# Kernel tuning notes

Measured on AMD Instinct MI355X. Metric: run time of the kernel, lower is better.

## Reference

```python
import jax, jax.numpy as jnp
import numpy as np

N_GRAPHS = 500
NODES_PER_GRAPH = 200
EDGES_PER_GRAPH = 6400
N = N_GRAPHS * NODES_PER_GRAPH          # 100000 nodes
E = N_GRAPHS * EDGES_PER_GRAPH          # 3200000 edges
D = 256                                  # dim_hidden
RATIO = 0.8
EPS = 1e-12


def setup_inputs() -> dict:
    key = jax.random.key(0)
    k1, k2 = jax.random.split(key, 2)
    x = jax.random.normal(k1, (N, D), dtype=jnp.float32)
    # edges consistent with batch: both endpoints inside the same graph
    rng = np.random.default_rng(0)
    g = np.repeat(np.arange(N_GRAPHS, dtype=np.int32), EDGES_PER_GRAPH)
    row = g * NODES_PER_GRAPH + rng.integers(0, NODES_PER_GRAPH, E).astype(np.int32)
    col = g * NODES_PER_GRAPH + rng.integers(0, NODES_PER_GRAPH, E).astype(np.int32)
    edge_index = jnp.asarray(np.stack([row, col]), dtype=jnp.int32)
    batch = jnp.asarray(np.repeat(np.arange(N_GRAPHS, dtype=np.int32), NODES_PER_GRAPH))
    W = jax.random.normal(k2, (2 * D, 1), dtype=jnp.float32) * (1.0 / np.sqrt(2 * D))
    b = jnp.zeros((1,), dtype=jnp.float32)
    return {"x": x, "edge_index": edge_index, "batch": batch, "W": W, "b": b}


def _edge_scores(x, W, b, edge_index):
    # concat(x[row], x[col]) @ W == (x @ W_row)[row] + (x @ W_col)[col]
    # -> avoids materializing the [E, 2D] edge_rep tensor.
    row, col = edge_index[0], edge_index[1]
    s_row = x @ W[:D, 0]   # [N]
    s_col = x @ W[D:, 0]   # [N]
    return s_row[row] + s_col[col] + b[0]  # [E]


def _topk_edge_mask(edge_score, edge_graph):
    # sparse_sort (descending=True): norm = minmax(score) - graph_id; argsort desc.
    f_min, f_max = edge_score.min(), edge_score.max()
    norm = (edge_score - f_min) / (f_max - f_min + EPS) - edge_graph.astype(edge_score.dtype)
    perm = jnp.argsort(-norm)  # graphs ascending, score descending within graph
    deg = jax.ops.segment_sum(jnp.ones_like(edge_graph), edge_graph, num_segments=N_GRAPHS)
    k = jnp.ceil(RATIO * deg.astype(jnp.float32)).astype(deg.dtype)
    start = jnp.concatenate([jnp.zeros((1,), deg.dtype), jnp.cumsum(deg)[:-1]])
    sg = edge_graph[perm]                        # graph id in sorted order
    pos = jnp.arange(E, dtype=deg.dtype) - start[sg]  # rank within segment
    keep_sorted = pos < k[sg]
    # scatter keep flags back to original edge order
    return jnp.zeros((E,), dtype=bool).at[perm].set(keep_sorted)


def _relabel(x, batch, edge_index, emask):
    # padded equivalent of torch.unique + scatter relabel:
    # selected nodes are compacted to the front of x/batch; dropped slots -> -1.
    row, col = edge_index[0], edge_index[1]
    m = emask.astype(jnp.int32)
    sel = (jnp.zeros((N,), jnp.int32).at[row].max(m).at[col].max(m)).astype(bool)
    new_id = jnp.where(sel, jnp.cumsum(sel) - 1, -1)           # [N]
    new_ei = jnp.where(emask[None, :], new_id[edge_index], -1)  # [2, E], -1 = padding
    order = jnp.argsort(~sel)                                   # stable: selected first
    x_out = x[order]                                            # [N, D], selected at front
    batch_out = jnp.where(sel[order], batch[order], -1)
    return x_out, new_ei, batch_out, sel.sum()


def reference(x, edge_index, batch, W, b):
    edge_score = _edge_scores(x, W, b, edge_index)
    edge_graph = batch[edge_index[0]]
    mask = _topk_edge_mask(edge_score, edge_graph)   # True = causal edge
    causal_w = jnp.where(mask, edge_score, 0.0)
    conf_w = jnp.where(mask, 0.0, -edge_score)
    causal_x, causal_ei, causal_batch, n_causal = _relabel(x, batch, edge_index, mask)
    conf_x, conf_ei, conf_batch, n_conf = _relabel(x, batch, edge_index, ~mask)
    return (causal_x, causal_ei, causal_w, causal_batch, n_causal,
            conf_x, conf_ei, conf_w, conf_batch, n_conf,
            edge_score, mask)
```

## Files before the change

### kernel.cpp

```cpp
#include <hip/hip_runtime.h>
#include <cmath>

typedef unsigned long long u64;
typedef unsigned int u32;
typedef unsigned char u8;

#define DHID 256
#define NMAX 100000
#define EMAX 3200000
#define EPGMAX 6400
#define NPG 200
#define GMAX 512
#define TOPK_T 1024

__device__ float  g_srow[NMAX];
__device__ float  g_scol[NMAX];
__device__ uchar2 g_lei[EMAX];
__device__ u8     g_mask[EMAX];
__device__ u8     g_selC[NMAX];
__device__ u8     g_selF[NMAX];
__device__ float  g_pmin[GMAX];
__device__ float  g_pmax[GMAX];
__device__ int    g_cntC[GMAX];
__device__ int    g_cntF[GMAX];
__device__ int    g_offC[GMAX];
__device__ int    g_offF[GMAX];
__device__ int    g_tot[2];

__global__ __launch_bounds__(256) void k_scores(const float* __restrict__ x,
    const int* __restrict__ ei, const float* __restrict__ W, const float* __restrict__ b,
    float* __restrict__ out, long long oS, int E, int N){
  __shared__ float srow_l[NPG], scol_l[NPG];
  __shared__ float smin[4], smax[4];
  int g = blockIdx.x, tid = threadIdx.x;
  int lane = tid & 63, wid = tid >> 6;
  int nbase = g * NPG;

  float4 wr = ((const float4*)W)[lane];
  float4 wc = ((const float4*)W)[64 + lane];
  for (int it = 0; it < NPG/4; it++){
    int n0 = it*4 + wid;
    int n = nbase + n0;
    float4 xv = ((const float4*)(x + (size_t)n*DHID))[lane];
    double dr = (double)xv.x*wr.x + (double)xv.y*wr.y + (double)xv.z*wr.z + (double)xv.w*wr.w;
    double dc = (double)xv.x*wc.x + (double)xv.y*wc.y + (double)xv.z*wc.z + (double)xv.w*wc.w;
    #pragma unroll
    for (int off = 32; off; off >>= 1){
      dr += __shfl_xor(dr, off);
      dc += __shfl_xor(dc, off);
    }
    if (lane == 0){ srow_l[n0] = (float)dr; scol_l[n0] = (float)dc; }
  }
  __syncthreads();
  if (tid < NPG){
    g_srow[nbase + tid] = srow_l[tid];
    g_scol[nbase + tid] = scol_l[tid];
  }

  float b0 = b[0];
  float lmin = INFINITY, lmax = -INFINITY;
  long long ebase = (long long)g * EPGMAX;
  for (int it = 0; it < EPGMAX/256; it++){
    long long e = ebase + it*256 + tid;
    int r0 = ei[e]     - nbase;
    int c0 = ei[E + e] - nbase;
    r0 = min(max(r0, 0), NPG-1);
    c0 = min(max(c0, 0), NPG-1);
    float s = (srow_l[r0] + scol_l[c0]) + b0;
    uchar2 rc; rc.x = (u8)r0; rc.y = (u8)c0;
    g_lei[e] = rc;
    out[oS + e] = s;
    lmin = fminf(lmin, s); lmax = fmaxf(lmax, s);
  }
  #pragma unroll
  for (int off = 32; off; off >>= 1){
    lmin = fminf(lmin, __shfl_xor(lmin, off));
    lmax = fmaxf(lmax, __shfl_xor(lmax, off));
  }
  if (lane == 0){ smin[wid] = lmin; smax[wid] = lmax; }
  __syncthreads();
  if (tid == 0){
    g_pmin[g] = fminf(fminf(smin[0], smin[1]), fminf(smin[2], smin[3]));
    g_pmax[g] = fmaxf(fmaxf(smax[0], smax[1]), fmaxf(smax[2], smax[3]));
  }
}

__global__ __launch_bounds__(TOPK_T) void k_topk(const float* __restrict__ b,
    float* __restrict__ out, long long oCW, long long oFW, long long oM,
    int E, int EPG, int k){
  __shared__ u32 keys[EPGMAX];
  __shared__ u8  keep[EPGMAX];
  __shared__ float srow_l[NPG], scol_l[NPG];
  __shared__ u8 selC_l[NPG], selF_l[NPG];
  __shared__ int hist[256];
  __shared__ float wred[16], wred2[16];
  __shared__ int wsum[16];
  __shared__ u32 sh_prefix;
  __shared__ int sh_rem, sh_rem_next, sh_digit;
  int g = blockIdx.x, tid = threadIdx.x;
  int lane = tid & 63, wid = tid >> 6;
  int G = (int)gridDim.x;
  int nbase = g * NPG;
  long long base = (long long)g * EPG;

  if (tid < NPG){
    srow_l[tid] = g_srow[nbase + tid];
    scol_l[tid] = g_scol[nbase + tid];
    selC_l[tid] = 0; selF_l[tid] = 0;
  }

  float lmin = (tid < G) ? g_pmin[tid] : INFINITY;
  float lmax = (tid < G) ? g_pmax[tid] : -INFINITY;
  #pragma unroll
  for (int off = 32; off; off >>= 1){
    lmin = fminf(lmin, __shfl_xor(lmin, off));
    lmax = fmaxf(lmax, __shfl_xor(lmax, off));
  }
  if (lane == 0){ wred[wid] = lmin; wred2[wid] = lmax; }
  if (tid == 0){ sh_prefix = 0; sh_rem = k; }
  __syncthreads();
  float fmin = wred[0], fmax = wred2[0];
  #pragma unroll
  for (int w = 1; w < 16; w++){
    fmin = fminf(fmin, wred[w]); fmax = fmaxf(fmax, wred2[w]);
  }

  float b0 = b[0];
  float denom = (fmax - fmin) + 1e-12f;
  float gf = (float)g;

  for (int i = tid; i < EPG; i += TOPK_T){
    uchar2 rc = g_lei[base + i];
    float s = (srow_l[rc.x] + scol_l[rc.y]) + b0;
    float frac = (s - fmin) / denom;
    float nk = frac - gf;
    u32 u = __float_as_uint(nk);
    u = (u & 0x80000000u) ? ~u : (u | 0x80000000u);
    keys[i] = ~u;
  }
  for (int shift = 24; shift >= 0; shift -= 8){
    if (tid < 256) hist[tid] = 0;
    __syncthreads();
    u32 pref = sh_prefix;
    for (int i = tid; i < EPG; i += TOPK_T){
      u32 kk = keys[i];
      bool cand = (shift == 24) || ((kk >> (shift + 8)) == pref);
      if (cand){
        u32 digit = (kk >> shift) & 0xFF;
        u32 d0 = __builtin_amdgcn_readfirstlane(digit);
        if (__all(digit == d0)){
          u64 m = __ballot(1);
          if (lane == __builtin_ctzll(m)) atomicAdd(&hist[d0], (int)__popcll(m));
        } else {
          atomicAdd(&hist[digit], 1);
        }
      }
    }
    __syncthreads();
    int v = 0, inc = 0;
    if (tid < 256){
      v = hist[tid];
      inc = v;
      #pragma unroll
      for (int off = 1; off < 64; off <<= 1){
        int t2 = __shfl_up(inc, off);
        if (lane >= off) inc += t2;
      }
      if (lane == 63) wsum[wid] = inc;
    }
    __syncthreads();
    if (tid < 256){
      int wpre = 0;
      for (int w = 0; w < wid; w++) wpre += wsum[w];
      int incl = inc + wpre;
      int cumprev = incl - v;
      int rem = sh_rem;
      if (cumprev < rem && rem <= incl){
        sh_digit = tid;
        sh_rem_next = rem - cumprev;
      }
    }
    __syncthreads();
    if (tid == 0){
      sh_prefix = (sh_prefix << 8) | (u32)sh_digit;
      sh_rem = sh_rem_next;
    }
    __syncthreads();
  }
  u32 T = sh_prefix;
  int r_budget = sh_rem;

  int CH = (EPG + TOPK_T - 1) / TOPK_T;
  int c0 = tid * CH;
  int cnt = 0;
  for (int j = 0; j < CH; j++){
    int i = c0 + j;
    if (i < EPG && keys[i] == T) cnt++;
  }
  int inc2 = cnt;
  #pragma unroll
  for (int off = 1; off < 64; off <<= 1){
    int t2 = __shfl_up(inc2, off);
    if (lane >= off) inc2 += t2;
  }
  if (lane == 63) wsum[wid] = inc2;
  __syncthreads();
  int wpre2 = 0;
  for (int w = 0; w < wid; w++) wpre2 += wsum[w];
  int rank = inc2 - cnt + wpre2;

  for (int j = 0; j < CH; j++){
    int i = c0 + j;
    if (i >= EPG) break;
    u32 kk = keys[i];
    int kept;
    if (kk < T) kept = 1;
    else if (kk == T){ kept = (rank < r_budget); rank++; }
    else kept = 0;
    keep[i] = (u8)kept;
  }
  __syncthreads();

  for (int i = tid; i < EPG; i += TOPK_T){
    long long e = base + i;
    int kept = keep[i];
    uchar2 rc = g_lei[e];
    float s = (srow_l[rc.x] + scol_l[rc.y]) + b0;
    g_mask[e] = (u8)kept;
    out[oM + e]  = kept ? 1.0f : 0.0f;
    out[oCW + e] = kept ? s : 0.0f;
    out[oFW + e] = kept ? 0.0f : -s;
    if (kept){ selC_l[rc.x] = 1; selC_l[rc.y] = 1; }
    else     { selF_l[rc.x] = 1; selF_l[rc.y] = 1; }
  }
  __syncthreads();

  if (tid < NPG){
    g_selC[nbase + tid] = selC_l[tid];
    g_selF[nbase + tid] = selF_l[tid];
  }
  if (tid < 256){
    int vC = (tid < NPG) ? (int)selC_l[tid] : 0;
    int vF = (tid < NPG) ? (int)selF_l[tid] : 0;
    #pragma unroll
    for (int off = 32; off; off >>= 1){
      vC += __shfl_xor(vC, off); vF += __shfl_xor(vF, off);
    }
    if (lane == 0){ wsum[wid] = vC; wsum[8 + wid] = vF; }
  }
  __syncthreads();
  if (tid == 0){
    g_cntC[g] = wsum[0]+wsum[1]+wsum[2]+wsum[3];
    g_cntF[g] = wsum[8]+wsum[9]+wsum[10]+wsum[11];
  }
}

__global__ __launch_bounds__(GMAX) void k_scan(int G, float* __restrict__ out,
    long long oNC, long long oNF){
  __shared__ int wsC[8], wsF[8];
  int tid = threadIdx.x;
  int lane = tid & 63, wid = tid >> 6;
  int c = (tid < G) ? g_cntC[tid] : 0;
  int f = (tid < G) ? g_cntF[tid] : 0;
  int ic = c, iff = f;
  #pragma unroll
  for (int off = 1; off < 64; off <<= 1){
    int a = __shfl_up(ic, off), b2 = __shfl_up(iff, off);
    if (lane >= off){ ic += a; iff += b2; }
  }
  if (lane == 63){ wsC[wid] = ic; wsF[wid] = iff; }
  __syncthreads();
  int pc = 0, pf = 0;
  for (int w = 0; w < wid; w++){ pc += wsC[w]; pf += wsF[w]; }
  if (tid < G){ g_offC[tid] = ic - c + pc; g_offF[tid] = iff - f + pf; }
  if (tid == GMAX - 1){
    g_tot[0] = ic + pc; g_tot[1] = iff + pf;
    out[oNC] = (float)(ic + pc);
    out[oNF] = (float)(iff + pf);
  }
}

__global__ __launch_bounds__(256) void k_final(const float* __restrict__ x,
    float* __restrict__ out, long long oCX, long long oFX, long long oCE, long long oFE,
    long long oCB, long long oFB, int E, int N, int EPG){
  __shared__ int dC_l[NPG], dF_l[NPG];
  __shared__ int wsC[4], wsF[4];
  int g = blockIdx.x, tid = threadIdx.x;
  int lane = tid & 63, wid = tid >> 6;
  int nbase = g * NPG;
  long long ebase = (long long)g * EPG;

  int sC = (tid < NPG) ? (int)g_selC[nbase + tid] : 0;
  int sF = (tid < NPG) ? (int)g_selF[nbase + tid] : 0;
  int ic = sC, iff = sF;
  #pragma unroll
  for (int off = 1; off < 64; off <<= 1){
    int a = __shfl_up(ic, off), b2 = __shfl_up(iff, off);
    if (lane >= off){ ic += a; iff += b2; }
  }
  if (lane == 63){ wsC[wid] = ic; wsF[wid] = iff; }
  __syncthreads();
  int pc = 0, pf = 0;
  for (int w = 0; w < wid; w++){ pc += wsC[w]; pf += wsF[w]; }
  int cumC = ic + pc;
  int cumF = iff + pf;
  int offC = g_offC[g], offF = g_offF[g];
  int nC = g_tot[0], nF = g_tot[1];
  if (tid < NPG){
    int n = nbase + tid;
    int gCumC = offC + cumC;
    int gCumF = offF + cumF;
    int dC = sC ? (gCumC - 1) : (nC + (n - gCumC));
    int dF = sF ? (gCumF - 1) : (nF + (n - gCumF));
    dC = min(max(dC, 0), N-1);
    dF = min(max(dF, 0), N-1);
    dC_l[tid] = dC; dF_l[tid] = dF;
    float bt = (float)g;
    out[oCB + dC] = sC ? bt : -1.0f;
    out[oFB + dF] = sF ? bt : -1.0f;
  }
  __syncthreads();

  for (int it = 0; it < EPGMAX/256; it++){
    long long e = ebase + it*256 + tid;
    uchar2 rc = g_lei[e];
    int m = g_mask[e];
    out[oCE + e]     = m ? (float)dC_l[rc.x] : -1.0f;
    out[oCE + E + e] = m ? (float)dC_l[rc.y] : -1.0f;
    out[oFE + e]     = m ? -1.0f : (float)dF_l[rc.x];
    out[oFE + E + e] = m ? -1.0f : (float)dF_l[rc.y];
  }

  for (int it = 0; it < NPG/4; it++){
    int t = it*4 + wid;
    int n = nbase + t;
    float4 v = ((const float4*)(x + (size_t)n*DHID))[lane];
    int dC = dC_l[t], dF = dF_l[t];
    *reinterpret_cast<float4*>(out + oCX + (long long)dC*DHID + lane*4) = v;
    long long iF = oFX + (long long)dF*DHID + lane*4;
    out[iF] = v.x;
    float2 mid; mid.x = v.y; mid.y = v.z;
    *reinterpret_cast<float2*>(out + iF + 1) = mid;
    out[iF + 3] = v.w;
  }
}

extern "C" void kernel_launch(void* const* d_in, const int* in_sizes, int n_in,
                              void* d_out, int out_size, void* d_ws, size_t ws_size,
                              hipStream_t stream) {
  const float* x   = (const float*)d_in[0];
  const int* ei    = (const int*)d_in[1];
  const float* W   = (const float*)d_in[3];
  const float* b   = (const float*)d_in[4];
  float* out = (float*)d_out;

  int N   = in_sizes[0] / DHID;
  int E   = in_sizes[1] / 2;
  if (N > NMAX) N = NMAX;
  if (E > EMAX) E = EMAX;
  const int G   = N / NPG;
  int EPG = (G > 0) ? E / G : 0;
  if (EPG > EPGMAX) EPG = EPGMAX;
  const int k   = (int)ceilf(0.8f * (float)EPG);

  long long oCX = 0;
  long long oCE = oCX + (long long)N*DHID;
  long long oCW = oCE + 2LL*E;
  long long oCB = oCW + E;
  long long oNC = oCB + N;
  long long oFX = oNC + 1;
  long long oFE = oFX + (long long)N*DHID;
  long long oFW = oFE + 2LL*E;
  long long oFB = oFW + E;
  long long oNF = oFB + N;
  long long oS  = oNF + 1;
  long long oM  = oS + E;

  k_scores<<<G, 256, 0, stream>>>(x, ei, W, b, out, oS, E, N);
  k_topk<<<G, TOPK_T, 0, stream>>>(b, out, oCW, oFW, oM, E, EPG, k);
  k_scan<<<1, GMAX, 0, stream>>>(G, out, oNC, oNF);
  k_final<<<G, 256, 0, stream>>>(x, out, oCX, oFX, oCE, oFE, oCB, oFB, E, N, EPG);
}
```

Measured before the change: 161.5 us.

## Fuse graph-offset scan into final kernel and skip common radix digits in top-k

Removes the single-block scan kernel: each final block now reduces all per-graph counts itself to get its exclusive offset and the global totals, saving a launch and a serialization point. The final kernel moves to 512 threads. In top-k, the per-graph key min/max is reduced and the radix select starts at the highest byte where min and max differ, skipping histogram passes over leading bytes that all keys share. Every final block redundantly reads and reduces the count arrays, which adds some work per block.

```diff
diff --git a/kernel.cpp b/kernel.cpp
--- a/kernel.cpp
+++ b/kernel.cpp
@@ -23,9 +23,6 @@
 __device__ float  g_pmax[GMAX];
 __device__ int    g_cntC[GMAX];
 __device__ int    g_cntF[GMAX];
-__device__ int    g_offC[GMAX];
-__device__ int    g_offF[GMAX];
-__device__ int    g_tot[2];
 
 __global__ __launch_bounds__(256) void k_scores(const float* __restrict__ x,
     const int* __restrict__ ei, const float* __restrict__ W, const float* __restrict__ b,
@@ -95,6 +92,7 @@
   __shared__ int hist[256];
   __shared__ float wred[16], wred2[16];
   __shared__ int wsum[16];
+  __shared__ u32 wkmin[16], wkmax[16];
   __shared__ u32 sh_prefix;
   __shared__ int sh_rem, sh_rem_next, sh_digit;
   int g = blockIdx.x, tid = threadIdx.x;
@@ -117,7 +115,6 @@
     lmax = fmaxf(lmax, __shfl_xor(lmax, off));
   }
   if (lane == 0){ wred[wid] = lmin; wred2[wid] = lmax; }
-  if (tid == 0){ sh_prefix = 0; sh_rem = k; }
   __syncthreads();
   float fmin = wred[0], fmax = wred2[0];
   #pragma unroll
@@ -129,6 +126,7 @@
   float denom = (fmax - fmin) + 1e-12f;
   float gf = (float)g;
 
+  u32 ukmin = 0xFFFFFFFFu, ukmax = 0u;
   for (int i = tid; i < EPG; i += TOPK_T){
     uchar2 rc = g_lei[base + i];
     float s = (srow_l[rc.x] + scol_l[rc.y]) + b0;
@@ -136,15 +134,41 @@
     float nk = frac - gf;
     u32 u = __float_as_uint(nk);
     u = (u & 0x80000000u) ? ~u : (u | 0x80000000u);
-    keys[i] = ~u;
-  }
-  for (int shift = 24; shift >= 0; shift -= 8){
+    u32 kk = ~u;
+    keys[i] = kk;
+    ukmin = min(ukmin, kk); ukmax = max(ukmax, kk);
+  }
+  #pragma unroll
+  for (int off = 32; off; off >>= 1){
+    ukmin = min(ukmin, (u32)__shfl_xor((int)ukmin, off));
+    ukmax = max(ukmax, (u32)__shfl_xor((int)ukmax, off));
+  }
+  if (lane == 0){ wkmin[wid] = ukmin; wkmax[wid] = ukmax; }
+  __syncthreads();
+  u32 kmin = wkmin[0], kmax = wkmax[0];
+  #pragma unroll
+  for (int w = 1; w < 16; w++){
+    kmin = min(kmin, wkmin[w]); kmax = max(kmax, wkmax[w]);
+  }
+
+  u32 diff = kmin ^ kmax;
+  int startShift; u32 prefInit;
+  if (diff == 0){ startShift = -8; prefInit = kmin; }
+  else {
+    int sb = (31 - __clz(diff)) >> 3;
+    startShift = sb * 8;
+    prefInit = (sb == 3) ? 0u : (kmin >> ((sb+1)*8));
+  }
+  if (tid == 0){ sh_prefix = prefInit; sh_rem = k; }
+  __syncthreads();
+
+  for (int shift = startShift; shift >= 0; shift -= 8){
     if (tid < 256) hist[tid] = 0;
     __syncthreads();
     u32 pref = sh_prefix;
     for (int i = tid; i < EPG; i += TOPK_T){
       u32 kk = keys[i];
-      bool cand = (shift == 24) || ((kk >> (shift + 8)) == pref);
+      bool cand = (shift == startShift) || ((kk >> (shift + 8)) == pref);
       if (cand){
         u32 digit = (kk >> shift) & 0xFF;
         u32 d0 = __builtin_amdgcn_readfirstlane(digit);
@@ -255,41 +279,39 @@
   }
 }
 
-__global__ __launch_bounds__(GMAX) void k_scan(int G, float* __restrict__ out,
-    long long oNC, long long oNF){
-  __shared__ int wsC[8], wsF[8];
-  int tid = threadIdx.x;
-  int lane = tid & 63, wid = tid >> 6;
-  int c = (tid < G) ? g_cntC[tid] : 0;
-  int f = (tid < G) ? g_cntF[tid] : 0;
-  int ic = c, iff = f;
-  #pragma unroll
-  for (int off = 1; off < 64; off <<= 1){
-    int a = __shfl_up(ic, off), b2 = __shfl_up(iff, off);
-    if (lane >= off){ ic += a; iff += b2; }
-  }
-  if (lane == 63){ wsC[wid] = ic; wsF[wid] = iff; }
-  __syncthreads();
-  int pc = 0, pf = 0;
-  for (int w = 0; w < wid; w++){ pc += wsC[w]; pf += wsF[w]; }
-  if (tid < G){ g_offC[tid] = ic - c + pc; g_offF[tid] = iff - f + pf; }
-  if (tid == GMAX - 1){
-    g_tot[0] = ic + pc; g_tot[1] = iff + pf;
-    out[oNC] = (float)(ic + pc);
-    out[oNF] = (float)(iff + pf);
-  }
-}
-
-__global__ __launch_bounds__(256) void k_final(const float* __restrict__ x,
+__global__ __launch_bounds__(512) void k_final(const float* __restrict__ x,
     float* __restrict__ out, long long oCX, long long oFX, long long oCE, long long oFE,
-    long long oCB, long long oFB, int E, int N, int EPG){
+    long long oCB, long long oFB, long long oNC, long long oNF,
+    int E, int N, int EPG, int G){
   __shared__ int dC_l[NPG], dF_l[NPG];
+  __shared__ int wredA[8], wredB[8], wredC2[8], wredD[8];
   __shared__ int wsC[4], wsF[4];
   int g = blockIdx.x, tid = threadIdx.x;
   int lane = tid & 63, wid = tid >> 6;
   int nbase = g * NPG;
   long long ebase = (long long)g * EPG;
 
+  int vC = (tid < G) ? g_cntC[tid] : 0;
+  int vF = (tid < G) ? g_cntF[tid] : 0;
+  int mC = (tid < g) ? vC : 0;
+  int mF = (tid < g) ? vF : 0;
+  #pragma unroll
+  for (int off = 32; off; off >>= 1){
+    vC += __shfl_xor(vC, off); vF += __shfl_xor(vF, off);
+    mC += __shfl_xor(mC, off); mF += __shfl_xor(mF, off);
+  }
+  if (lane == 0){ wredA[wid] = vC; wredB[wid] = vF; wredC2[wid] = mC; wredD[wid] = mF; }
+  __syncthreads();
+  int nC = 0, nF = 0, offC = 0, offF = 0;
+  #pragma unroll
+  for (int w = 0; w < 8; w++){
+    nC += wredA[w]; nF += wredB[w]; offC += wredC2[w]; offF += wredD[w];
+  }
+  if (g == 0 && tid == 0){
+    out[oNC] = (float)nC;
+    out[oNF] = (float)nF;
+  }
+
   int sC = (tid < NPG) ? (int)g_selC[nbase + tid] : 0;
   int sF = (tid < NPG) ? (int)g_selF[nbase + tid] : 0;
   int ic = sC, iff = sF;
@@ -298,18 +320,14 @@
     int a = __shfl_up(ic, off), b2 = __shfl_up(iff, off);
     if (lane >= off){ ic += a; iff += b2; }
   }
-  if (lane == 63){ wsC[wid] = ic; wsF[wid] = iff; }
-  __syncthreads();
-  int pc = 0, pf = 0;
-  for (int w = 0; w < wid; w++){ pc += wsC[w]; pf += wsF[w]; }
-  int cumC = ic + pc;
-  int cumF = iff + pf;
-  int offC = g_offC[g], offF = g_offF[g];
-  int nC = g_tot[0], nF = g_tot[1];
+  if (lane == 63 && wid < 4){ wsC[wid] = ic; wsF[wid] = iff; }
+  __syncthreads();
   if (tid < NPG){
+    int pc = 0, pf = 0;
+    for (int w = 0; w < wid; w++){ pc += wsC[w]; pf += wsF[w]; }
+    int gCumC = offC + ic + pc;
+    int gCumF = offF + iff + pf;
     int n = nbase + tid;
-    int gCumC = offC + cumC;
-    int gCumF = offF + cumF;
     int dC = sC ? (gCumC - 1) : (nC + (n - gCumC));
     int dF = sF ? (gCumF - 1) : (nF + (n - gCumF));
     dC = min(max(dC, 0), N-1);
@@ -321,8 +339,8 @@
   }
   __syncthreads();
 
-  for (int it = 0; it < EPGMAX/256; it++){
-    long long e = ebase + it*256 + tid;
+  for (int i = tid; i < EPG; i += 512){
+    long long e = ebase + i;
     uchar2 rc = g_lei[e];
     int m = g_mask[e];
     out[oCE + e]     = m ? (float)dC_l[rc.x] : -1.0f;
@@ -331,8 +349,8 @@
     out[oFE + E + e] = m ? -1.0f : (float)dF_l[rc.y];
   }
 
-  for (int it = 0; it < NPG/4; it++){
-    int t = it*4 + wid;
+  for (int it = 0; it < NPG/8; it++){
+    int t = it*8 + wid;
     int n = nbase + t;
     float4 v = ((const float4*)(x + (size_t)n*DHID))[lane];
     int dC = dC_l[t], dF = dF_l[t];
@@ -378,6 +396,5 @@
 
   k_scores<<<G, 256, 0, stream>>>(x, ei, W, b, out, oS, E, N);
   k_topk<<<G, TOPK_T, 0, stream>>>(b, out, oCW, oFW, oM, E, EPG, k);
-  k_scan<<<1, GMAX, 0, stream>>>(G, out, oNC, oNF);
-  k_final<<<G, 256, 0, stream>>>(x, out, oCX, oFX, oCE, oFE, oCB, oFB, E, N, EPG);
+  k_final<<<G, 512, 0, stream>>>(x, out, oCX, oFX, oCE, oFE, oCB, oFB, oNC, oNF, E, N, EPG, G);
 }
```

New measurement: 156.5 us, median of 2. -3.1%, faster.
